# Performance work log

Measured on AMD Instinct MI355X. Metric: run time of the kernel, lower is better.

Reference implementation:

```python
import jax, jax.numpy as jnp
import numpy as np

B, N, D, H, E, S, K, O = 32, 4096, 64, 64, 65536, 2, 2, 128
F = D + H                      # input_size = input_dim + hid_dim
M = S * K + 1                  # num_matrices


def setup_inputs() -> dict:
    key = jax.random.key(0)
    ks = jax.random.split(key, 7)
    inputs = jax.random.normal(ks[0], (B, N * D), dtype=jnp.float32)
    state = jax.random.normal(ks[1], (B, N * H), dtype=jnp.float32)
    # two sparse random-walk supports in COO form (rows, cols, vals)
    sup_rows = jax.random.randint(ks[2], (S, E), 0, N, dtype=jnp.int32)
    sup_cols = jax.random.randint(ks[3], (S, E), 0, N, dtype=jnp.int32)
    sup_vals = jax.random.uniform(ks[4], (S, E), dtype=jnp.float32) / 16.0
    # xavier_normal_ with gain=1.414
    std = 1.414 * np.sqrt(2.0 / (F * M + O))
    weight = jax.random.normal(ks[5], (F * M, O), dtype=jnp.float32) * std
    biases = jnp.zeros((O,), dtype=jnp.float32)  # bias_start = 0.0
    return {"inputs": inputs, "state": state, "sup_rows": sup_rows,
            "sup_cols": sup_cols, "sup_vals": sup_vals,
            "weight": weight, "biases": biases, "output_size": O}


def reference(inputs, state, sup_rows, sup_cols, sup_vals, weight, biases, output_size):
    b = inputs.shape[0]
    x_in = inputs.reshape(b, N, -1)
    st = state.reshape(b, N, -1)
    x = jnp.concatenate([x_in, st], axis=2)          # [B, N, F]
    f = x.shape[2]
    # [B,N,F] -> [N,F,B] -> [N, F*B]
    x0 = jnp.transpose(x, (1, 2, 0)).reshape(N, f * b)

    def spmm(s, m):
        # y[r] += v * m[c]  (sparse support @ dense)
        return jax.ops.segment_sum(sup_vals[s][:, None] * m[sup_cols[s]],
                                   sup_rows[s], num_segments=N)

    xs = [x0]
    for s in range(sup_vals.shape[0]):
        x1 = spmm(s, x0)
        xs.append(x1)
        xk_1, xk_2 = x1, x0
        for _ in range(2, K + 1):
            x2 = 2.0 * spmm(s, xk_1) - xk_2   # Chebyshev recurrence
            xs.append(x2)
            xk_1, xk_2 = x2, xk_1

    m = len(xs)
    # [M,N,F*B] -> [M,N,F,B] -> [B,N,F,M] -> [B*N, F*M]
    xc = jnp.stack(xs).reshape(m, N, f, b)
    xc = jnp.transpose(xc, (3, 1, 2, 0)).reshape(b * N, f * m)
    out = xc @ weight + biases                       # [B*N, O]
    return out.reshape(b, N * output_size)
```

## Files before the change

kernel.cpp:

```cpp
#include <hip/hip_runtime.h>
#include <hip/hip_bf16.h>

#define Bv 32
#define Nv 4096
#define Dv 64
#define Hv 64
#define Fv 128
#define Ev 65536
#define Sv 2
#define Ov 128
#define Mv 5

typedef unsigned int uint;
using short8  = __attribute__((ext_vector_type(8))) short;
using floatx4 = __attribute__((ext_vector_type(4))) float;
using f32x2   = __attribute__((ext_vector_type(2))) float;
using uintx4  = __attribute__((ext_vector_type(4))) uint;

#define AS1 __attribute__((address_space(1)))
#define AS3 __attribute__((address_space(3)))

__device__ __forceinline__ float bflo(uint u){ uint v = u << 16; float f; __builtin_memcpy(&f, &v, 4); return f; }
__device__ __forceinline__ float bfhi(uint u){ uint v = u & 0xffff0000u; float f; __builtin_memcpy(&f, &v, 4); return f; }
__device__ __forceinline__ unsigned short f2bf(float f){
  uint x; __builtin_memcpy(&x, &f, 4);
  x += 0x7fffu + ((x >> 16) & 1u);
  return (unsigned short)(x >> 16);
}
__device__ __forceinline__ uint bfpack(float a, float b){
  return (uint)f2bf(a) | ((uint)f2bf(b) << 16);
}

__device__ __forceinline__ void ld16(void* lds, const void* g){
  __builtin_amdgcn_global_load_lds((const AS1 uint*)g, (AS3 uint*)lds, 16, 0, 0);
}

__global__ void k_zero(int* __restrict__ p, int n){
  int i = blockIdx.x * 256 + threadIdx.x;
  if(i < n) p[i] = 0;
}

__global__ void k_hist(const int* __restrict__ rows, int* __restrict__ deg){
  int i = blockIdx.x * 256 + threadIdx.x;
  int s = i >> 16;
  int r = rows[i];
  atomicAdd(&deg[s * Nv + r], 1);
}

__global__ void k_scan(const int* __restrict__ deg, int* __restrict__ rowptr, int* __restrict__ cursor){
  __shared__ int part[256];
  __shared__ int sbase[256];
  int t = threadIdx.x;
  for(int s = 0; s < Sv; s++){
    int loc[16]; int sum = 0;
    #pragma unroll
    for(int i = 0; i < 16; i++){ loc[i] = deg[s * Nv + t * 16 + i]; sum += loc[i]; }
    part[t] = sum;
    __syncthreads();
    if(t == 0){ int run = 0; for(int i = 0; i < 256; i++){ int v = part[i]; sbase[i] = run; run += v; } }
    __syncthreads();
    int run = sbase[t];
    #pragma unroll
    for(int i = 0; i < 16; i++){
      int idx = t * 16 + i;
      rowptr[s * (Nv + 1) + idx] = run;
      cursor[s * Nv + idx] = run;
      run += loc[i];
    }
    if(t == 255) rowptr[s * (Nv + 1) + Nv] = run;
    __syncthreads();
  }
}

__global__ void k_scatter(const int* __restrict__ rows, const int* __restrict__ cols,
                          const float* __restrict__ vals, int* __restrict__ cursor,
                          uint* __restrict__ pk){
  int i = blockIdx.x * 256 + threadIdx.x;
  int s = i >> 16;
  int r = rows[i];
  int p = atomicAdd(&cursor[s * Nv + r], 1);
  pk[(s << 16) + p] = (uint)cols[i] | ((uint)f2bf(vals[i]) << 16);
}

__global__ void k_buildx0(const float* __restrict__ inp, const float* __restrict__ st,
                          uint* __restrict__ X0bf, uint* __restrict__ X08){
  const int t = blockIdx.x * 256 + threadIdx.x;
  const int c = t & 7;
  const int n = (t >> 3) & (Nv - 1);
  const int b = t >> 15;
  const float* src = (c < 4) ? (inp + ((size_t)b * Nv + n) * 64 + c * 16)
                             : (st  + ((size_t)b * Nv + n) * 64 + (c - 4) * 16);
  float v[16];
  #pragma unroll
  for(int q = 0; q < 4; q++){
    float4 f4 = *(const float4*)(src + q * 4);
    v[q * 4 + 0] = f4.x; v[q * 4 + 1] = f4.y; v[q * 4 + 2] = f4.z; v[q * 4 + 3] = f4.w;
  }
  const size_t base = (size_t)b * Nv + n;
  uint bfw[8];
  #pragma unroll
  for(int q = 0; q < 8; q++) bfw[q] = bfpack(v[2 * q], v[2 * q + 1]);
  *(uintx4*)(X0bf + base * 64 + c * 8)     = *(uintx4*)(bfw);
  *(uintx4*)(X0bf + base * 64 + c * 8 + 4) = *(uintx4*)(bfw + 4);
  uint f8w[4];
  #pragma unroll
  for(int q = 0; q < 4; q++){
    int w = __builtin_amdgcn_cvt_pk_fp8_f32(v[4 * q + 0], v[4 * q + 1], 0, false);
    w     = __builtin_amdgcn_cvt_pk_fp8_f32(v[4 * q + 2], v[4 * q + 3], w, true);
    f8w[q] = (uint)w;
  }
  *(uintx4*)(X08 + base * 32 + c * 4) = *(uintx4*)(f8w);
}

__global__ void k_wb(const float* __restrict__ wg, unsigned short* __restrict__ Wb){
  int t = blockIdx.x * 256 + threadIdx.x;
  if(t >= Mv * Ov * Fv) return;
  int f = t & (Fv - 1);
  int o = (t >> 7) & (Ov - 1);
  int m = t >> 14;
  Wb[t] = f2bf(wg[(f * Mv + m) * Ov + o]);
}

__launch_bounds__(256)
__global__ void k_spmm3(const uint* __restrict__ src8,
                        uint* __restrict__ dstA, uint* __restrict__ dstB,
                        uint* __restrict__ dA8, uint* __restrict__ dB8,
                        const uint* __restrict__ xprev,
                        const int* __restrict__ rowptr, const uint* __restrict__ pk,
                        const int two_supports){
  const int lane = threadIdx.x & 63;
  const int wv   = threadIdx.x >> 6;
  int bid = blockIdx.x;
  int s = 0;
  if(two_supports){ s = bid >> 12; bid &= 4095; }
  const int pg = bid & 3;
  const int r  = (bid >> 2) * 4 + wv;
  const int p  = pg * 8 + (lane >> 3);
  const int cB = (lane & 7) * 16;
  const int* rp   = rowptr + s * (Nv + 1);
  const uint* pks = pk + (s << 16);
  const int j0 = rp[r], j1 = rp[r + 1];
  const uint* gb = src8 + (size_t)p * Nv * 32 + (cB >> 2);
  uint* dst = s ? dstB : dstA;
  uint* d8  = s ? dB8  : dA8;

  float acc[16];
  #pragma unroll
  for(int k = 0; k < 16; k++) acc[k] = 0.f;

  for(int j = j0; j < j1; j += 64){
    int rem = j1 - j; if(rem > 64) rem = 64;
    const uint e = (lane < rem) ? pks[j + lane] : 0u;
    for(int t = 0; t < rem; t += 8){
      uintx4 g[8]; float v[8];
      #pragma unroll
      for(int u = 0; u < 8; u++){
        const uint eu = __shfl(e, t + u, 64);
        v[u] = bfhi(eu);
        const uint col = eu & 0xffffu;
        g[u] = *(const uintx4*)(gb + (size_t)col * 32);
      }
      #pragma unroll
      for(int u = 0; u < 8; u++){
        #pragma unroll
        for(int d = 0; d < 4; d++){
          f32x2 lo = __builtin_amdgcn_cvt_pk_f32_fp8((int)g[u][d], false);
          f32x2 hi = __builtin_amdgcn_cvt_pk_f32_fp8((int)g[u][d], true);
          acc[d * 4 + 0] += v[u] * lo[0];
          acc[d * 4 + 1] += v[u] * lo[1];
          acc[d * 4 + 2] += v[u] * hi[0];
          acc[d * 4 + 3] += v[u] * hi[1];
        }
      }
    }
  }

  const size_t obase = (size_t)p * Nv + r;
  if(xprev){
    const uint* pv = xprev + obase * 64 + (cB >> 1);
    uint pw[8];
    *(uintx4*)(pw)     = *(const uintx4*)(pv);
    *(uintx4*)(pw + 4) = *(const uintx4*)(pv + 4);
    #pragma unroll
    for(int q = 0; q < 8; q++){
      acc[2 * q + 0] = 2.f * acc[2 * q + 0] - bflo(pw[q]);
      acc[2 * q + 1] = 2.f * acc[2 * q + 1] - bfhi(pw[q]);
    }
  }
  uint bfw[8];
  #pragma unroll
  for(int q = 0; q < 8; q++) bfw[q] = bfpack(acc[2 * q], acc[2 * q + 1]);
  uint* db = dst + obase * 64 + (cB >> 1);
  __builtin_nontemporal_store(*(uintx4*)(bfw),     (uintx4*)(db));
  __builtin_nontemporal_store(*(uintx4*)(bfw + 4), (uintx4*)(db + 4));
  if(d8){
    uint f8w[4];
    #pragma unroll
    for(int q = 0; q < 4; q++){
      int w = __builtin_amdgcn_cvt_pk_fp8_f32(acc[4 * q + 0], acc[4 * q + 1], 0, false);
      w     = __builtin_amdgcn_cvt_pk_fp8_f32(acc[4 * q + 2], acc[4 * q + 3], w, true);
      f8w[q] = (uint)w;
    }
    __builtin_nontemporal_store(*(uintx4*)(f8w), (uintx4*)(d8 + obase * 32 + (cB >> 2)));
  }
}

__launch_bounds__(256)
__global__ void k_gemm(const unsigned short* __restrict__ X0,
                       const unsigned short* __restrict__ X1a,
                       const unsigned short* __restrict__ X2a,
                       const unsigned short* __restrict__ X1b,
                       const unsigned short* __restrict__ X2b,
                       const unsigned short* __restrict__ Wb,
                       const float* __restrict__ bias,
                       float* __restrict__ out){
  __shared__ unsigned short Asm[128 * 32];
  __shared__ unsigned short Bsm[128 * 32];
  const unsigned short* Am[5] = {X0, X1a, X2a, X1b, X2b};
  const int tid  = threadIdx.x;
  const int lane = tid & 63, wv = tid >> 6;
  const int wm = wv >> 1, wn = wv & 1;
  const int lrow = lane & 15, quad = lane >> 4;
  const size_t r0 = (size_t)blockIdx.x * 128;

  floatx4 acc[4][4] = {};

  #pragma unroll
  for(int m = 0; m < 5; m++){
    const unsigned short* Ab = Am[m] + r0 * Fv;
    const unsigned short* Bb = Wb + m * (Ov * Fv);
    #pragma unroll
    for(int kk = 0; kk < Fv; kk += 32){
      __syncthreads();
      #pragma unroll
      for(int p = 0; p < 2; p++){
        const int base_idx = p * 256 + wv * 64;
        const int my_idx = base_idx + lane;
        const int row = my_idx >> 2, seg = my_idx & 3;
        ld16(&Asm[base_idx * 8], Ab + (size_t)row * Fv + kk + seg * 8);
        ld16(&Bsm[base_idx * 8], Bb + row * Fv + kk + seg * 8);
      }
      __syncthreads();
      short8 af[4], bfr[4];
      #pragma unroll
      for(int t = 0; t < 4; t++){
        af[t]  = *(const short8*)(&Asm[(wm * 64 + t * 16 + lrow) * 32 + quad * 8]);
        bfr[t] = *(const short8*)(&Bsm[(wn * 64 + t * 16 + lrow) * 32 + quad * 8]);
      }
      #pragma unroll
      for(int ti = 0; ti < 4; ti++)
        #pragma unroll
        for(int tj = 0; tj < 4; tj++)
          acc[ti][tj] = __builtin_amdgcn_mfma_f32_16x16x32_bf16(af[ti], bfr[tj], acc[ti][tj], 0, 0, 0);
    }
  }

  #pragma unroll
  for(int ti = 0; ti < 4; ti++){
    #pragma unroll
    for(int tj = 0; tj < 4; tj++){
      const int col = wn * 64 + tj * 16 + lrow;
      const float bv = bias[col];
      const size_t rbase = r0 + wm * 64 + ti * 16 + quad * 4;
      #pragma unroll
      for(int t = 0; t < 4; t++){
        out[(rbase + t) * Ov + col] = acc[ti][tj][t] + bv;
      }
    }
  }
}

extern "C" void kernel_launch(void* const* d_in, const int* in_sizes, int n_in,
                              void* d_out, int out_size, void* d_ws, size_t ws_size,
                              hipStream_t stream) {
  (void)in_sizes; (void)n_in; (void)out_size; (void)ws_size;
  const float* inp  = (const float*)d_in[0];
  const float* st   = (const float*)d_in[1];
  const int*   rows = (const int*)d_in[2];
  const int*   cols = (const int*)d_in[3];
  const float* vals = (const float*)d_in[4];
  const float* wght = (const float*)d_in[5];
  const float* bias = (const float*)d_in[6];
  float* out = (float*)d_out;

  char* w = (char*)d_ws;
  const size_t SZX  = (size_t)Bv * Nv * Fv * 2;
  const size_t SZX8 = (size_t)Bv * Nv * Fv;
  unsigned short* X0  = (unsigned short*)(w);
  unsigned short* X1a = (unsigned short*)(w + SZX);
  unsigned short* X2a = (unsigned short*)(w + 2 * SZX);
  unsigned short* X1b = (unsigned short*)(w + 3 * SZX);
  unsigned short* X2b = (unsigned short*)(w + 4 * SZX);
  uint* X08  = (uint*)(w + 5 * SZX);
  uint* X1a8 = (uint*)(w + 5 * SZX + SZX8);
  uint* X1b8 = (uint*)(w + 5 * SZX + 2 * SZX8);
  unsigned short* Wb = (unsigned short*)(w + 5 * SZX + 3 * SZX8);
  char* p2 = w + 5 * SZX + 3 * SZX8 + 262144;
  int* deg    = (int*)p2;
  int* cursor = deg + Sv * Nv;
  int* rowptr = cursor + Sv * Nv;
  uint* pk    = (uint*)(rowptr + Sv * (Nv + 1) + 62);

  k_zero<<<(Sv * Nv + 255) / 256, 256, 0, stream>>>(deg, Sv * Nv);
  k_hist<<<Sv * Ev / 256, 256, 0, stream>>>(rows, deg);
  k_scan<<<1, 256, 0, stream>>>(deg, rowptr, cursor);
  k_scatter<<<Sv * Ev / 256, 256, 0, stream>>>(rows, cols, vals, cursor, pk);
  k_buildx0<<<(Bv * Nv * 8) / 256, 256, 0, stream>>>(inp, st, (uint*)X0, X08);
  k_wb<<<(Mv * Ov * Fv + 255) / 256, 256, 0, stream>>>(wght, Wb);

  k_spmm3<<<8192, 256, 0, stream>>>(X08, (uint*)X1a, (uint*)X1b, X1a8, X1b8,
                                    (const uint*)nullptr, rowptr, pk, 1);
  k_spmm3<<<4096, 256, 0, stream>>>(X1a8, (uint*)X2a, (uint*)X2a, nullptr, nullptr,
                                    (const uint*)X0, rowptr, pk, 0);
  k_spmm3<<<4096, 256, 0, stream>>>(X1b8, (uint*)X2b, (uint*)X2b, nullptr, nullptr,
                                    (const uint*)X0, rowptr + (Nv + 1), pk + Ev, 0);

  k_gemm<<<(Bv * Nv) / 128, 256, 0, stream>>>(X0, X1a, X2a, X1b, X2b, Wb, bias, out);
}
```

Before: 339.0 us.

## Restructure GEMM: stage whole weight slice in LDS, load A directly to registers

The GEMM kernel now loads the full 128x128 bf16 weight slice for each matrix into shared memory in one pass, with a pre-swizzled layout, instead of staging 32-wide K chunks of both A and B. Each wave owns 32 rows across all 128 output columns and reads its A fragments straight from global memory into registers. This cuts the number of barriers per matrix from eight to two and removes A traffic through LDS. The output stores become nontemporal. In exchange, the A loads no longer go through LDS, so global latency is less hidden, and the accumulator footprint per wave changes shape.

```diff
diff --git a/kernel.cpp b/kernel.cpp
--- a/kernel.cpp
+++ b/kernel.cpp
@@ -214,58 +214,62 @@
                        const unsigned short* __restrict__ Wb,
                        const float* __restrict__ bias,
                        float* __restrict__ out){
-  __shared__ unsigned short Asm[128 * 32];
-  __shared__ unsigned short Bsm[128 * 32];
+  __shared__ uint Wsm[8192];
   const unsigned short* Am[5] = {X0, X1a, X2a, X1b, X2b};
   const int tid  = threadIdx.x;
   const int lane = tid & 63, wv = tid >> 6;
-  const int wm = wv >> 1, wn = wv & 1;
   const int lrow = lane & 15, quad = lane >> 4;
   const size_t r0 = (size_t)blockIdx.x * 128;
-
-  floatx4 acc[4][4] = {};
+  const int rowbase = wv * 32;
+
+  floatx4 acc[2][8] = {};
+
+  int woff[8];
+  #pragma unroll
+  for(int q = 0; q < 8; q++){
+    const int X = (q * 4 + wv) * 1024 + lane * 16;
+    const int c = X >> 13, rem = X & 8191;
+    const int o = rem >> 6, qd = (rem >> 4) & 3;
+    woff[q] = o * 256 + c * 64 + qd * 16;
+  }
 
   #pragma unroll
   for(int m = 0; m < 5; m++){
-    const unsigned short* Ab = Am[m] + r0 * Fv;
-    const unsigned short* Bb = Wb + m * (Ov * Fv);
-    #pragma unroll
-    for(int kk = 0; kk < Fv; kk += 32){
-      __syncthreads();
-      #pragma unroll
-      for(int p = 0; p < 2; p++){
-        const int base_idx = p * 256 + wv * 64;
-        const int my_idx = base_idx + lane;
-        const int row = my_idx >> 2, seg = my_idx & 3;
-        ld16(&Asm[base_idx * 8], Ab + (size_t)row * Fv + kk + seg * 8);
-        ld16(&Bsm[base_idx * 8], Bb + row * Fv + kk + seg * 8);
-      }
-      __syncthreads();
-      short8 af[4], bfr[4];
-      #pragma unroll
-      for(int t = 0; t < 4; t++){
-        af[t]  = *(const short8*)(&Asm[(wm * 64 + t * 16 + lrow) * 32 + quad * 8]);
-        bfr[t] = *(const short8*)(&Bsm[(wn * 64 + t * 16 + lrow) * 32 + quad * 8]);
-      }
-      #pragma unroll
-      for(int ti = 0; ti < 4; ti++)
+    const unsigned short* Ab = Am[m] + (r0 + rowbase) * Fv;
+    const char* Wm = (const char*)(Wb + m * (Ov * Fv));
+    __syncthreads();
+    #pragma unroll
+    for(int q = 0; q < 8; q++){
+      ld16((char*)Wsm + (q * 4 + wv) * 1024, Wm + woff[q]);
+    }
+    __syncthreads();
+    #pragma unroll
+    for(int kk = 0; kk < 4; kk++){
+      short8 af[2], bfr[8];
+      #pragma unroll
+      for(int t = 0; t < 2; t++)
+        af[t] = *(const short8*)(Ab + (size_t)(t * 16 + lrow) * Fv + kk * 32 + quad * 8);
+      #pragma unroll
+      for(int j = 0; j < 8; j++)
+        bfr[j] = *(const short8*)((const char*)Wsm + kk * 8192 + (j * 16 + lrow) * 64 + quad * 16);
+      #pragma unroll
+      for(int t = 0; t < 2; t++)
         #pragma unroll
-        for(int tj = 0; tj < 4; tj++)
-          acc[ti][tj] = __builtin_amdgcn_mfma_f32_16x16x32_bf16(af[ti], bfr[tj], acc[ti][tj], 0, 0, 0);
-    }
-  }
-
-  #pragma unroll
-  for(int ti = 0; ti < 4; ti++){
-    #pragma unroll
-    for(int tj = 0; tj < 4; tj++){
-      const int col = wn * 64 + tj * 16 + lrow;
+        for(int j = 0; j < 8; j++)
+          acc[t][j] = __builtin_amdgcn_mfma_f32_16x16x32_bf16(af[t], bfr[j], acc[t][j], 0, 0, 0);
+    }
+  }
+
+  #pragma unroll
+  for(int t = 0; t < 2; t++){
+    const size_t rb = r0 + rowbase + t * 16 + quad * 4;
+    #pragma unroll
+    for(int j = 0; j < 8; j++){
+      const int col = j * 16 + lrow;
       const float bv = bias[col];
-      const size_t rbase = r0 + wm * 64 + ti * 16 + quad * 4;
-      #pragma unroll
-      for(int t = 0; t < 4; t++){
-        out[(rbase + t) * Ov + col] = acc[ti][tj][t] + bv;
-      }
+      #pragma unroll
+      for(int g = 0; g < 4; g++)
+        __builtin_nontemporal_store(acc[t][j][g] + bv, out + (rb + g) * Ov + col);
     }
   }
 }
```

After: 346.1 us. +2.1%, slower.
